# Optimization experiments

Hardware: AMD Instinct MI355X
Metric: run time of the kernel (lower is better)

## Reference

```python
import jax, jax.numpy as jnp
import numpy as np
from jax import lax

EPS = 1e-5
HEADS = 4
NPOINT = 512


def _layernorm(x, g, b):
    mu = jnp.mean(x, axis=-1, keepdims=True)
    var = jnp.var(x, axis=-1, keepdims=True)
    return (x - mu) * lax.rsqrt(var + EPS) * g + b


def farthest_point_sample(xyz, npoint):
    # xyz: [B, N, 3] -> idx [B, npoint]  (canonical PointNet++ FPS, seeded at point 0)
    B, N, _ = xyz.shape

    def step(carry, _):
        dist, far = carry  # [B,N], [B]
        centroid = jnp.take_along_axis(xyz, far[:, None, None], axis=1)  # [B,1,3]
        d = jnp.sum((xyz - centroid) ** 2, axis=-1)  # [B,N]
        dist = jnp.minimum(dist, d)
        nxt = jnp.argmax(dist, axis=1).astype(jnp.int32)
        return (dist, nxt), far

    init = (jnp.full((B, N), 1e10, xyz.dtype), jnp.zeros((B,), jnp.int32))
    _, idx = lax.scan(step, init, None, length=npoint)  # [npoint, B]
    return idx.T  # [B, npoint]


def index_points(points, idx):
    # points: [B, N, D], idx: [B, S] -> [B, S, D]
    return jnp.take_along_axis(points, idx[..., None], axis=1)


def setup_inputs() -> dict:
    key = jax.random.key(0)
    ks = iter(jax.random.split(key, 16))
    B, N, Cin, D, Dff, Dout = 8, 2048, 64, 128, 512, 256
    w = lambda k, s: (jax.random.normal(k, s, jnp.float32) * 0.02)
    inp = {
        "xyz": jax.random.normal(next(ks), (B, 3, N), jnp.float32),
        "points": jax.random.normal(next(ks), (B, Cin, N), jnp.float32),
        "W_proj": w(next(ks), (D, Cin)), "b_proj": jnp.zeros((D,)),
        "bn1_g": jnp.ones((D,)), "bn1_b": jnp.zeros((D,)),
        "bn1_m": jnp.zeros((D,)), "bn1_v": jnp.ones((D,)),
        "W_pos": w(next(ks), (D, 3)), "b_pos": jnp.zeros((D,)),
        "Wq": w(next(ks), (D, D)), "bq": jnp.zeros((D,)),
        "Wk": w(next(ks), (D, D)), "bk": jnp.zeros((D,)),
        "Wv": w(next(ks), (D, D)), "bv": jnp.zeros((D,)),
        "Wo": w(next(ks), (D, D)), "bo": jnp.zeros((D,)),
        "ln1_g": jnp.ones((D,)), "ln1_b": jnp.zeros((D,)),
        "W1": w(next(ks), (Dff, D)), "b1": jnp.zeros((Dff,)),
        "W2": w(next(ks), (D, Dff)), "b2": jnp.zeros((D,)),
        "ln2_g": jnp.ones((D,)), "ln2_b": jnp.zeros((D,)),
        "W_fc": w(next(ks), (Dout, D + 3)), "b_fc": jnp.zeros((Dout,)),
        "bn2_g": jnp.ones((Dout,)), "bn2_b": jnp.zeros((Dout,)),
        "bn2_m": jnp.zeros((Dout,)), "bn2_v": jnp.ones((Dout,)),
    }
    return inp


def reference(xyz, points, W_proj, b_proj, bn1_g, bn1_b, bn1_m, bn1_v,
              W_pos, b_pos, Wq, bq, Wk, bk, Wv, bv, Wo, bo,
              ln1_g, ln1_b, W1, b1, W2, b2, ln2_g, ln2_b,
              W_fc, b_fc, bn2_g, bn2_b, bn2_m, bn2_v):
    B, _, N = xyz.shape
    D = W_proj.shape[0]
    hd = D // HEADS

    # project: pointwise conv + BN (inference), output [B, N, D]
    feat = jnp.einsum('dc,bcn->bnd', W_proj, points) + b_proj
    feat = (feat - bn1_m) * lax.rsqrt(bn1_v + EPS) * bn1_g + bn1_b

    # transformer block with xyz positional encoding
    pos = jnp.einsum('dc,bcn->bnd', W_pos, xyz) + b_pos
    x = feat + pos
    q = (x @ Wq.T + bq).reshape(B, N, HEADS, hd)
    k = (x @ Wk.T + bk).reshape(B, N, HEADS, hd)
    v = (x @ Wv.T + bv).reshape(B, N, HEADS, hd)
    scores = jnp.einsum('bnhd,bmhd->bhnm', q, k) / jnp.sqrt(jnp.float32(hd))
    attn = jax.nn.softmax(scores, axis=-1)
    o = jnp.einsum('bhnm,bmhd->bnhd', attn, v).reshape(B, N, D)
    x = _layernorm(x + (o @ Wo.T + bo), ln1_g, ln1_b)
    ffn = jax.nn.relu(x @ W1.T + b1) @ W2.T + b2
    features = _layernorm(x + ffn, ln2_g, ln2_b)  # [B, N, D]

    # sampling + gather
    xyz_t = jnp.transpose(xyz, (0, 2, 1))  # [B, N, 3]
    fps_idx = farthest_point_sample(xyz_t, NPOINT)  # [B, npoint]
    new_points = index_points(features, fps_idx)    # [B, npoint, D]
    new_xyz = index_points(xyz_t, fps_idx)          # [B, npoint, 3]

    cat = jnp.concatenate([new_points, new_xyz], axis=-1)  # [B, npoint, D+3]
    out = jnp.einsum('od,bnd->bon', W_fc, cat) + b_fc[None, :, None]
    out = (out - bn2_m[None, :, None]) * lax.rsqrt(bn2_v + EPS)[None, :, None] \
          * bn2_g[None, :, None] + bn2_b[None, :, None]
    out = jax.nn.relu(out)  # [B, Dout, npoint]

    return jnp.transpose(new_xyz, (0, 2, 1)), out
```

## Files before the change

kernel.cpp:

```cpp
#include <hip/hip_runtime.h>
#include <hip/hip_bf16.h>

#define B_    8
#define N_    2048
#define CIN_  64
#define D_    128
#define DFF_  512
#define DOUT_ 256
#define S_    512
#define H_    4
#define HD_   32
#define EPS_  1e-5f

typedef unsigned short u16;
typedef unsigned long long u64;
typedef __attribute__((ext_vector_type(8))) short short8v;
typedef __attribute__((ext_vector_type(4))) float f32x4;

__device__ __forceinline__ u16 f2bu(float f) {
  __hip_bfloat16 h = __float2bfloat16(f);
  return *(u16*)&h;
}
__device__ __forceinline__ float bu2f(u16 u) {
  __hip_bfloat16 h = *(__hip_bfloat16*)&u;
  return __bfloat162float(h);
}

#define OW_QKV 0
#define OW_O   49152
#define OW_1   65536
#define OW_2   131072
#define OW_FC  196608
#define OW_CAT 237568
#define NW_TOT 249856

__global__ __launch_bounds__(256) void prep_kernel(
    const float* __restrict__ Wq, const float* __restrict__ bq,
    const float* __restrict__ Wk, const float* __restrict__ bk,
    const float* __restrict__ Wv, const float* __restrict__ bv,
    const float* __restrict__ Wo, const float* __restrict__ W1,
    const float* __restrict__ W2, const float* __restrict__ Wfc,
    const float* __restrict__ bfc, const float* __restrict__ Wp,
    const float* __restrict__ bp, const float* __restrict__ Wpos,
    const float* __restrict__ bpos, const float* __restrict__ g1,
    const float* __restrict__ be1, const float* __restrict__ m1,
    const float* __restrict__ v1, const float* __restrict__ g2,
    const float* __restrict__ bb2, const float* __restrict__ m2,
    const float* __restrict__ v2, u16* __restrict__ wb,
    float* __restrict__ fb) {
  const float SC = 0.1767766952966369f * 1.4426950408889634f;
  int i = blockIdx.x * 256 + threadIdx.x;
  if (i < OW_O) {
    int n = i >> 7, k = i & 127;
    float v = (n < 128) ? Wq[i] * SC
                        : (n < 256) ? Wk[(n - 128) * 128 + k]
                                    : Wv[(n - 256) * 128 + k];
    wb[OW_QKV + i] = f2bu(v);
  } else if (i < OW_1) {
    wb[i] = f2bu(Wo[i - OW_O]);
  } else if (i < OW_2) {
    wb[i] = f2bu(W1[i - OW_1]);
  } else if (i < OW_FC) {
    wb[i] = f2bu(W2[i - OW_2]);
  } else if (i < OW_CAT) {
    int j = i - OW_FC;
    int n = j / 160, c = j % 160;
    wb[i] = f2bu(c < 131 ? Wfc[n * 131 + c] : 0.f);
  } else if (i < NW_TOT) {
    int j = i - OW_CAT;
    int d = j / 96, c = j % 96;
    float v;
    if (c < 64) v = Wp[d * 64 + c] * (g1[d] * rsqrtf(v1[d] + EPS_));
    else if (c < 67) v = Wpos[d * 3 + (c - 64)];
    else v = 0.f;
    wb[i] = f2bu(v);
  } else if (i < NW_TOT + 384) {
    int n = i - NW_TOT;
    fb[n] = (n < 128) ? bq[n] * SC : (n < 256) ? bk[n - 128] : bv[n - 256];
  } else if (i < NW_TOT + 512) {
    int d = i - (NW_TOT + 384);
    float s1 = g1[d] * rsqrtf(v1[d] + EPS_);
    fb[384 + d] = (bp[d] - m1[d]) * s1 + be1[d] + bpos[d];
  } else if (i < NW_TOT + 768) {
    int n = i - (NW_TOT + 512);
    fb[512 + n] = g2[n] * rsqrtf(v2[n] + EPS_);
  } else if (i < NW_TOT + 1024) {
    int n = i - (NW_TOT + 768);
    float s = g2[n] * rsqrtf(v2[n] + EPS_);
    fb[768 + n] = bfc[n] * s + bb2[n] - m2[n] * s;
  }
}

#define FPS_SMEM 320

template <int CTRL, int RM>
__device__ __forceinline__ float dppmax(float v) {
  int m = __builtin_amdgcn_update_dpp(__float_as_int(v), __float_as_int(v),
                                      CTRL, RM, 0xF, true);
  return fmaxf(v, __int_as_float(m));
}

__device__ __forceinline__ void fps_slice(
    char* smem, int b, const float* __restrict__ xyz,
    float* __restrict__ dist_ws, int* __restrict__ far_ws,
    int* __restrict__ idx_out, float* __restrict__ out0, int s0, int s1) {
  u64* keys = (u64*)smem;
  float* crd = (float*)(smem + 64);
  __builtin_amdgcn_s_setprio(3);
  const int t = threadIdx.x, w = t >> 6, lane = t & 63;
  const float* xb = xyz + (size_t)b * 3 * N_;
  const int base = (w * 64 + lane) * 8;
  float* dw = dist_ws + b * N_;
  float px[8], py[8], pz[8], dist[8];
#pragma unroll
  for (int j = 0; j < 8; j++) {
    px[j] = xb[base + j];
    py[j] = xb[N_ + base + j];
    pz[j] = xb[2 * N_ + base + j];
    dist[j] = 1e10f;
  }
  if (s0 != 0) {
#pragma unroll
    for (int j = 0; j < 8; j++) dist[j] = dw[base + j];
  }
  int far = (s0 == 0) ? 0 : far_ws[b];
  float cx = xb[far], cy = xb[N_ + far], cz = xb[2 * N_ + far];
  for (int s = s0; s < s1; s++) {
    if (t == 0) {
      idx_out[b * S_ + s] = far;
      out0[(size_t)b * 3 * S_ + s] = cx;
      out0[(size_t)b * 3 * S_ + S_ + s] = cy;
      out0[(size_t)b * 3 * S_ + 2 * S_ + s] = cz;
    }
    float best = -1.0f, bx = 0.f, by = 0.f, bz = 0.f;
    int bestp = 0;
#pragma unroll
    for (int j = 0; j < 8; j++) {
      float dx = __fsub_rn(px[j], cx);
      float dy = __fsub_rn(py[j], cy);
      float dz = __fsub_rn(pz[j], cz);
      float d = __fadd_rn(__fadd_rn(__fmul_rn(dx, dx), __fmul_rn(dy, dy)),
                          __fmul_rn(dz, dz));
      float nd = fminf(dist[j], d);
      dist[j] = nd;
      if (nd > best) {
        best = nd; bestp = base + j;
        bx = px[j]; by = py[j]; bz = pz[j];
      }
    }
    float m = best;
    m = dppmax<0x111, 0xF>(m);
    m = dppmax<0x112, 0xF>(m);
    m = dppmax<0x114, 0xF>(m);
    m = dppmax<0x118, 0xF>(m);
    m = dppmax<0x142, 0xA>(m);
    m = dppmax<0x143, 0xC>(m);
    float M = __int_as_float(__builtin_amdgcn_readlane(__float_as_int(m), 63));
    u64 mask = __ballot(best == M);
    int wl = __ffsll((long long)mask) - 1;
    if (lane == wl) {
      int sb = (s & 1) * 4 + w;
      keys[sb] = ((u64)__float_as_uint(M) << 32) |
                 (unsigned)(0xFFFFFFFFu - (unsigned)bestp);
      crd[sb * 3 + 0] = bx;
      crd[sb * 3 + 1] = by;
      crd[sb * 3 + 2] = bz;
    }
    asm volatile("s_waitcnt lgkmcnt(0)" ::: "memory");
    __builtin_amdgcn_s_barrier();
    asm volatile("" ::: "memory");
    const int q0 = (s & 1) * 4;
    u64 kk = keys[q0];
    float ccx = crd[q0 * 3], ccy = crd[q0 * 3 + 1], ccz = crd[q0 * 3 + 2];
#pragma unroll
    for (int i = 1; i < 4; i++) {
      u64 ki = keys[q0 + i];
      bool c = ki > kk;
      kk = c ? ki : kk;
      ccx = c ? crd[(q0 + i) * 3] : ccx;
      ccy = c ? crd[(q0 + i) * 3 + 1] : ccy;
      ccz = c ? crd[(q0 + i) * 3 + 2] : ccz;
    }
    far = (int)(0xFFFFFFFFu - (unsigned)kk);
    cx = ccx; cy = ccy; cz = ccz;
  }
#pragma unroll
  for (int j = 0; j < 8; j++) dw[base + j] = dist[j];
  if (t == 0) far_ws[b] = far;
  __builtin_amdgcn_s_setprio(0);
}

template <int K, int KC, int ASTAGE, int EPI>
__global__ __launch_bounds__(256) void gemm_k(
    const u16* __restrict__ A, const u16* __restrict__ W,
    const float* __restrict__ srcf0, const float* __restrict__ srcf1,
    const int* __restrict__ fidx, const float* __restrict__ p0,
    const float* __restrict__ p1, const float* __restrict__ p2,
    const u16* __restrict__ resid, u16* __restrict__ outb,
    float* __restrict__ outf, int ntn, int fpsnb, int s0, int s1,
    const float* fxyz, float* fdist, int* ffar, int* fidxo, float* fout0) {
  constexpr int KP = KC + 8;
  constexpr int GEMM_SMEM = 2 * 128 * KP * 2;
  constexpr int SMEM = GEMM_SMEM > FPS_SMEM ? GEMM_SMEM : FPS_SMEM;
  __shared__ __align__(16) char smem[SMEM];
  if ((int)blockIdx.x < fpsnb) {
    fps_slice(smem, blockIdx.x, fxyz, fdist, ffar, fidxo, fout0, s0, s1);
    return;
  }
  u16 (*As)[KP] = (u16 (*)[KP])smem;
  u16 (*Ws)[KP] = (u16 (*)[KP])(smem + 128 * KP * 2);
  const int bid = blockIdx.x - fpsnb;
  const int mt = bid / ntn, nt = bid % ntn;
  const int t = threadIdx.x, w = t >> 6, lane = t & 63;
  const int g = lane >> 4, lr = lane & 15;

  f32x4 acc[2][8];
#pragma unroll
  for (int qf = 0; qf < 2; qf++)
#pragma unroll
    for (int nf = 0; nf < 8; nf++) acc[qf][nf] = {0.f, 0.f, 0.f, 0.f};

  for (int kc = 0; kc < K / KC; kc++) {
    __syncthreads();
    for (int i = t; i < 128 * (KC / 8); i += 256) {
      int row = i / (KC / 8), c8 = i % (KC / 8);
      *(short8v*)&Ws[row][c8 * 8] =
          *(const short8v*)(W + (size_t)(nt * 128 + row) * K + kc * KC + c8 * 8);
    }
    if constexpr (ASTAGE == 0) {
      for (int i = t; i < 128 * (KC / 8); i += 256) {
        int row = i / (KC / 8), c8 = i % (KC / 8);
        *(short8v*)&As[row][c8 * 8] =
            *(const short8v*)(A + (size_t)(mt * 128 + row) * K + kc * KC + c8 * 8);
      }
    } else if constexpr (ASTAGE == 1) {
      int bb = (mt * 128) >> 11, n0 = (mt * 128) & (N_ - 1);
      for (int i = t; i < 96 * 128; i += 256) {
        int c = i >> 7, n = i & 127;
        float v;
        if (c < 64) v = srcf0[((size_t)bb * CIN_ + c) * N_ + n0 + n];
        else if (c < 67) v = srcf1[((size_t)bb * 3 + (c - 64)) * N_ + n0 + n];
        else v = 0.f;
        As[n][c] = f2bu(v);
      }
    } else {
      int bb = (mt * 128) >> 9, sq0 = (mt * 128) & (S_ - 1);
      for (int i = t; i < 128 * 20; i += 256) {
        int row = i / 20, c8 = i % 20;
        int id = fidx[bb * S_ + sq0 + row];
        short8v val;
        if (c8 < 16) {
          val = *(const short8v*)(A + ((size_t)bb * N_ + id) * D_ + c8 * 8);
        } else if (c8 == 16) {
          val = short8v{0, 0, 0, 0, 0, 0, 0, 0};
          val[0] = (short)f2bu(srcf1[((size_t)bb * 3 + 0) * N_ + id]);
          val[1] = (short)f2bu(srcf1[((size_t)bb * 3 + 1) * N_ + id]);
          val[2] = (short)f2bu(srcf1[((size_t)bb * 3 + 2) * N_ + id]);
        } else {
          val = short8v{0, 0, 0, 0, 0, 0, 0, 0};
        }
        *(short8v*)&As[row][c8 * 8] = val;
      }
    }
    __syncthreads();
#pragma unroll
    for (int ks = 0; ks < KC / 32; ks++) {
      short8v a0 = *(const short8v*)&As[w * 32 + lr][ks * 32 + 8 * g];
      short8v a1 = *(const short8v*)&As[w * 32 + 16 + lr][ks * 32 + 8 * g];
#pragma unroll
      for (int nf = 0; nf < 8; nf++) {
        short8v bb = *(const short8v*)&Ws[nf * 16 + lr][ks * 32 + 8 * g];
        acc[0][nf] = __builtin_amdgcn_mfma_f32_16x16x32_bf16(a0, bb, acc[0][nf], 0, 0, 0);
        acc[1][nf] = __builtin_amdgcn_mfma_f32_16x16x32_bf16(a1, bb, acc[1][nf], 0, 0, 0);
      }
    }
  }

  if constexpr (EPI == 3) {
#pragma unroll
    for (int qf = 0; qf < 2; qf++) {
#pragma unroll
      for (int i = 0; i < 4; i++) {
        int m = mt * 128 + w * 32 + qf * 16 + 4 * g + i;
        float v[8], sm = 0.f, sq = 0.f;
#pragma unroll
        for (int nf = 0; nf < 8; nf++) {
          int n = nf * 16 + lr;
          float x = acc[qf][nf][i] + p0[n] + bu2f(resid[(size_t)m * D_ + n]);
          v[nf] = x;
          sm += x;
          sq += x * x;
        }
#pragma unroll
        for (int msk = 1; msk < 16; msk <<= 1) {
          sm += __shfl_xor(sm, msk);
          sq += __shfl_xor(sq, msk);
        }
        float mu = sm * (1.f / 128.f);
        float var = sq * (1.f / 128.f) - mu * mu;
        float rs = rsqrtf(var + EPS_);
#pragma unroll
        for (int nf = 0; nf < 8; nf++) {
          int n = nf * 16 + lr;
          outb[(size_t)m * D_ + n] = f2bu((v[nf] - mu) * rs * p1[n] + p2[n]);
        }
      }
    }
  } else {
#pragma unroll
    for (int qf = 0; qf < 2; qf++)
#pragma unroll
      for (int nf = 0; nf < 8; nf++)
#pragma unroll
        for (int i = 0; i < 4; i++) {
          int m = mt * 128 + w * 32 + qf * 16 + 4 * g + i;
          int nl = nf * 16 + lr;
          int n = nt * 128 + nl;
          float vv = acc[qf][nf][i];
          if constexpr (EPI == 0) {
            outb[(size_t)m * D_ + nl] = f2bu(vv + p0[n]);
          } else if constexpr (EPI == 1) {
            vv += p0[n];
            int which = n >> 7, h = (n >> 5) & 3, c = n & 31;
            int bb = m >> 11, tok = m & (N_ - 1);
            outb[(size_t)which * 2097152 +
                 (((size_t)bb * H_ + h) * N_ + tok) * HD_ + c] = f2bu(vv);
          } else if constexpr (EPI == 2) {
            outb[(size_t)m * DFF_ + n] = f2bu(fmaxf(vv + p0[n], 0.f));
          } else {
            float r = fmaxf(vv * p1[n] + p2[n], 0.f);
            outf[((size_t)(m >> 9) * DOUT_ + n) * S_ + (m & (S_ - 1))] = r;
          }
        }
  }
}

__global__ __launch_bounds__(256) void attn_mfma_kernel(
    const u16* __restrict__ qg, const u16* __restrict__ kg,
    const u16* __restrict__ vg, u16* __restrict__ o, int fpsnb, int s0, int s1,
    const float* fxyz, float* fdist, int* ffar, int* fidxo, float* fout0) {
  constexpr int ATTN_SMEM = 64 * 40 * 2 + 32 * 72 * 2 + 4 * 16 * 72 * 2;
  constexpr int SMEM = ATTN_SMEM > FPS_SMEM ? ATTN_SMEM : FPS_SMEM;
  __shared__ __align__(16) char smem[SMEM];
  if ((int)blockIdx.x < fpsnb) {
    fps_slice(smem, blockIdx.x, fxyz, fdist, ffar, fidxo, fout0, s0, s1);
    return;
  }
  const int t = threadIdx.x;
  const int w = t >> 6, lane = t & 63, g = lane >> 4, lr = lane & 15;
  u16 (*ks)[40] = (u16 (*)[40])smem;
  u16 (*vt)[72] = (u16 (*)[72])(smem + 5120);
  u16 (*psw)[72] = (u16 (*)[72])(smem + 9728) + w * 16;

  const int bid = blockIdx.x - fpsnb;
  const int qt = bid & 31;
  const int bh = bid >> 5;
  const int b = bh >> 2, h = bh & 3;
  const int qrow = qt * 64 + w * 16 + lr;

  short8v aq = *(const short8v*)(qg + ((size_t)bh * N_ + qrow) * HD_ + 8 * g);

  const u16* kb = kg + (size_t)bh * N_ * HD_;
  const u16* vb = vg + (size_t)bh * N_ * HD_;

  const f32x4 fzero = {0.f, 0.f, 0.f, 0.f};
  float mrun = -INFINITY, lrun = 0.f;
  f32x4 acco[2] = {fzero, fzero};

  const int srow = t >> 2, scol = (t & 3) * 8;

  for (int ch = 0; ch < 32; ch++) {
    __syncthreads();
    short8v kvv = *(const short8v*)(kb + (size_t)(ch * 64 + srow) * HD_ + scol);
    short8v vvv = *(const short8v*)(vb + (size_t)(ch * 64 + srow) * HD_ + scol);
    *(short8v*)(&ks[srow][scol]) = kvv;
#pragma unroll
    for (int e = 0; e < 8; e++) vt[scol + e][srow] = (u16)vvv[e];
    __syncthreads();

    f32x4 stv[4];
#pragma unroll
    for (int kt = 0; kt < 4; kt++) {
      short8v ak = *(const short8v*)(&ks[kt * 16 + lr][8 * g]);
      stv[kt] = __builtin_amdgcn_mfma_f32_16x16x32_bf16(ak, aq, fzero, 0, 0, 0);
    }

    float mx = -INFINITY;
#pragma unroll
    for (int kt = 0; kt < 4; kt++)
#pragma unroll
      for (int i = 0; i < 4; i++) mx = fmaxf(mx, stv[kt][i]);
    mx = fmaxf(mx, __shfl_xor(mx, 16));
    mx = fmaxf(mx, __shfl_xor(mx, 32));
    float nm = fmaxf(mrun, mx);
    float alpha = exp2f(mrun - nm);
    mrun = nm;
    float psum = 0.f;
#pragma unroll
    for (int kt = 0; kt < 4; kt++) {
      float p0 = exp2f(stv[kt][0] - nm);
      float p1 = exp2f(stv[kt][1] - nm);
      float p2 = exp2f(stv[kt][2] - nm);
      float p3 = exp2f(stv[kt][3] - nm);
      psum += (p0 + p1) + (p2 + p3);
      u64 pk = (u64)f2bu(p0) | ((u64)f2bu(p1) << 16) |
               ((u64)f2bu(p2) << 32) | ((u64)f2bu(p3) << 48);
      *(u64*)(&psw[lr][kt * 16 + 4 * g]) = pk;
    }
    psum += __shfl_xor(psum, 16);
    psum += __shfl_xor(psum, 32);
    lrun = lrun * alpha + psum;
#pragma unroll
    for (int dt = 0; dt < 2; dt++)
#pragma unroll
      for (int i = 0; i < 4; i++) acco[dt][i] *= alpha;

#pragma unroll
    for (int mc = 0; mc < 2; mc++) {
      short8v pb = *(const short8v*)(&psw[lr][mc * 32 + 8 * g]);
#pragma unroll
      for (int dt = 0; dt < 2; dt++) {
        short8v av = *(const short8v*)(&vt[dt * 16 + lr][mc * 32 + 8 * g]);
        acco[dt] = __builtin_amdgcn_mfma_f32_16x16x32_bf16(av, pb, acco[dt], 0, 0, 0);
      }
    }
  }

  float rl = 1.0f / lrun;
#pragma unroll
  for (int dt = 0; dt < 2; dt++) {
    u64 pk = (u64)f2bu(acco[dt][0] * rl) | ((u64)f2bu(acco[dt][1] * rl) << 16) |
             ((u64)f2bu(acco[dt][2] * rl) << 32) |
             ((u64)f2bu(acco[dt][3] * rl) << 48);
    *(u64*)(o + ((size_t)b * N_ + qrow) * D_ + h * HD_ + dt * 16 + 4 * g) = pk;
  }
}

extern "C" void kernel_launch(void* const* d_in, const int* in_sizes, int n_in,
                              void* d_out, int out_size, void* d_ws, size_t ws_size,
                              hipStream_t stream) {
  const float* xyz    = (const float*)d_in[0];
  const float* points = (const float*)d_in[1];
  const float* Wp     = (const float*)d_in[2];
  const float* bp     = (const float*)d_in[3];
  const float* g1     = (const float*)d_in[4];
  const float* be1    = (const float*)d_in[5];
  const float* m1     = (const float*)d_in[6];
  const float* v1     = (const float*)d_in[7];
  const float* Wpos   = (const float*)d_in[8];
  const float* bpos   = (const float*)d_in[9];
  const float* Wq     = (const float*)d_in[10];
  const float* bq     = (const float*)d_in[11];
  const float* Wk     = (const float*)d_in[12];
  const float* bk     = (const float*)d_in[13];
  const float* Wv     = (const float*)d_in[14];
  const float* bv     = (const float*)d_in[15];
  const float* Wo     = (const float*)d_in[16];
  const float* bo     = (const float*)d_in[17];
  const float* lg1    = (const float*)d_in[18];
  const float* lb1    = (const float*)d_in[19];
  const float* W1     = (const float*)d_in[20];
  const float* b1     = (const float*)d_in[21];
  const float* W2     = (const float*)d_in[22];
  const float* b2p    = (const float*)d_in[23];
  const float* lg2    = (const float*)d_in[24];
  const float* lb2    = (const float*)d_in[25];
  const float* Wfc    = (const float*)d_in[26];
  const float* bfc    = (const float*)d_in[27];
  const float* g2     = (const float*)d_in[28];
  const float* bb2    = (const float*)d_in[29];
  const float* m2     = (const float*)d_in[30];
  const float* v2     = (const float*)d_in[31];

  float* out0 = (float*)d_out;
  float* out1 = out0 + (size_t)B_ * 3 * S_;

  char* ws = (char*)d_ws;
  int*   fps_idx = (int*)ws;
  u16*   wb      = (u16*)(ws + 16384);
  float* fb      = (float*)(ws + 516096);
  float* dist_ws = (float*)(ws + 520192);
  int*   far_ws  = (int*)(ws + 585728);
  const size_t MB = 1024 * 1024;
  u16* x     = (u16*)(ws + 1 * MB);
  u16* o     = (u16*)(ws + 5 * MB);
  u16* x2    = (u16*)(ws + 9 * MB);
  u16* feats = (u16*)(ws + 13 * MB);
  u16* qb    = (u16*)(ws + 17 * MB);
  u16* h     = (u16*)(ws + 29 * MB);

  prep_kernel<<<980, 256, 0, stream>>>(Wq, bq, Wk, bk, Wv, bv, Wo, W1, W2, Wfc,
                                       bfc, Wp, bp, Wpos, bpos, g1, be1, m1, v1,
                                       g2, bb2, m2, v2, wb, fb);

  gemm_k<96, 96, 1, 0><<<8 + 128, 256, 0, stream>>>(
      nullptr, wb + OW_CAT, points, xyz, nullptr, fb + 384, nullptr, nullptr,
      nullptr, x, nullptr, 1, 8, 0, 48, xyz, dist_ws, far_ws, fps_idx, out0);
  gemm_k<128, 128, 0, 1><<<8 + 384, 256, 0, stream>>>(
      x, wb + OW_QKV, nullptr, nullptr, nullptr, fb, nullptr, nullptr,
      nullptr, qb, nullptr, 3, 8, 48, 136, xyz, dist_ws, far_ws, fps_idx, out0);
  attn_mfma_kernel<<<8 + B_ * H_ * (N_ / 64), 256, 0, stream>>>(
      qb, qb + 2097152, qb + 2 * 2097152, o, 8, 136, 236, xyz, dist_ws, far_ws,
      fps_idx, out0);
  gemm_k<128, 128, 0, 3><<<8 + 128, 256, 0, stream>>>(
      o, wb + OW_O, nullptr, nullptr, nullptr, bo, lg1, lb1, x, x2, nullptr, 1,
      8, 236, 320, xyz, dist_ws, far_ws, fps_idx, out0);
  gemm_k<128, 128, 0, 2><<<8 + 512, 256, 0, stream>>>(
      x2, wb + OW_1, nullptr, nullptr, nullptr, b1, nullptr, nullptr,
      nullptr, h, nullptr, 4, 8, 320, 420, xyz, dist_ws, far_ws, fps_idx, out0);
  gemm_k<512, 128, 0, 3><<<8 + 128, 256, 0, stream>>>(
      h, wb + OW_2, nullptr, nullptr, nullptr, b2p, lg2, lb2, x2, feats,
      nullptr, 1, 8, 420, 512, xyz, dist_ws, far_ws, fps_idx, out0);
  gemm_k<160, 160, 2, 4><<<64, 256, 0, stream>>>(
      feats, wb + OW_FC, nullptr, xyz, fps_idx, nullptr, fb + 512, fb + 768,
      nullptr, nullptr, out1, 2, 0, 0, 0, nullptr, nullptr, nullptr, nullptr,
      nullptr);
}
```

Measured before the change: 397.5 us.

## Store V transposed from QKV GEMM, drop FPS priority, rebalance FPS slices

After: 385.1 us. 1.03x faster.

```diff
diff --git a/kernel.cpp b/kernel.cpp
--- a/kernel.cpp
+++ b/kernel.cpp
@@ -106,7 +106,6 @@
     int* __restrict__ idx_out, float* __restrict__ out0, int s0, int s1) {
   u64* keys = (u64*)smem;
   float* crd = (float*)(smem + 64);
-  __builtin_amdgcn_s_setprio(3);
   const int t = threadIdx.x, w = t >> 6, lane = t & 63;
   const float* xb = xyz + (size_t)b * 3 * N_;
   const int base = (w * 64 + lane) * 8;
@@ -187,7 +186,6 @@
 #pragma unroll
   for (int j = 0; j < 8; j++) dw[base + j] = dist[j];
   if (t == 0) far_ws[b] = far;
-  __builtin_amdgcn_s_setprio(0);
 }
 
 template <int K, int KC, int ASTAGE, int EPI>
@@ -306,6 +304,44 @@
         }
       }
     }
+  } else if constexpr (EPI == 1) {
+    if (nt < 2) {
+#pragma unroll
+      for (int qf = 0; qf < 2; qf++)
+#pragma unroll
+        for (int nf = 0; nf < 8; nf++)
+#pragma unroll
+          for (int i = 0; i < 4; i++) {
+            int m = mt * 128 + w * 32 + qf * 16 + 4 * g + i;
+            int n = nt * 128 + nf * 16 + lr;
+            float vv = acc[qf][nf][i] + p0[n];
+            int hh = (n >> 5) & 3, c = n & 31;
+            int bb = m >> 11, tok = m & (N_ - 1);
+            outb[(size_t)nt * 2097152 +
+                 (((size_t)bb * H_ + hh) * N_ + tok) * HD_ + c] = f2bu(vv);
+          }
+    } else {
+      __syncthreads();
+      u16 (*Vt)[KP] = (u16 (*)[KP])smem;
+#pragma unroll
+      for (int qf = 0; qf < 2; qf++)
+#pragma unroll
+        for (int nf = 0; nf < 8; nf++)
+#pragma unroll
+          for (int i = 0; i < 4; i++) {
+            int m_l = w * 32 + qf * 16 + 4 * g + i;
+            int n_l = nf * 16 + lr;
+            Vt[n_l][m_l] = f2bu(acc[qf][nf][i] + p0[256 + n_l]);
+          }
+      __syncthreads();
+      int bb = (mt * 128) >> 11, tok0 = (mt * 128) & (N_ - 1);
+      for (int i2 = t; i2 < 2048; i2 += 256) {
+        int row = i2 >> 4, seg = i2 & 15;
+        *(short8v*)(outb + (size_t)2 * 2097152 +
+                    (((size_t)bb * H_ + (row >> 5)) * HD_ + (row & 31)) * N_ +
+                    tok0 + seg * 8) = *(const short8v*)&Vt[row][seg * 8];
+      }
+    }
   } else {
 #pragma unroll
     for (int qf = 0; qf < 2; qf++)
@@ -319,12 +355,6 @@
           float vv = acc[qf][nf][i];
           if constexpr (EPI == 0) {
             outb[(size_t)m * D_ + nl] = f2bu(vv + p0[n]);
-          } else if constexpr (EPI == 1) {
-            vv += p0[n];
-            int which = n >> 7, h = (n >> 5) & 3, c = n & 31;
-            int bb = m >> 11, tok = m & (N_ - 1);
-            outb[(size_t)which * 2097152 +
-                 (((size_t)bb * H_ + h) * N_ + tok) * HD_ + c] = f2bu(vv);
           } else if constexpr (EPI == 2) {
             outb[(size_t)m * DFF_ + n] = f2bu(fmaxf(vv + p0[n], 0.f));
           } else {
@@ -361,21 +391,21 @@
   short8v aq = *(const short8v*)(qg + ((size_t)bh * N_ + qrow) * HD_ + 8 * g);
 
   const u16* kb = kg + (size_t)bh * N_ * HD_;
-  const u16* vb = vg + (size_t)bh * N_ * HD_;
+  const u16* vbt = vg + (size_t)bh * N_ * HD_;
 
   const f32x4 fzero = {0.f, 0.f, 0.f, 0.f};
   float mrun = -INFINITY, lrun = 0.f;
   f32x4 acco[2] = {fzero, fzero};
 
-  const int srow = t >> 2, scol = (t & 3) * 8;
+  const int krow = t >> 2, kseg = (t & 3) * 8;
+  const int vrow = t >> 3, vseg = (t & 7) * 8;
 
   for (int ch = 0; ch < 32; ch++) {
     __syncthreads();
-    short8v kvv = *(const short8v*)(kb + (size_t)(ch * 64 + srow) * HD_ + scol);
-    short8v vvv = *(const short8v*)(vb + (size_t)(ch * 64 + srow) * HD_ + scol);
-    *(short8v*)(&ks[srow][scol]) = kvv;
-#pragma unroll
-    for (int e = 0; e < 8; e++) vt[scol + e][srow] = (u16)vvv[e];
+    *(short8v*)(&ks[krow][kseg]) =
+        *(const short8v*)(kb + (size_t)(ch * 64 + krow) * HD_ + kseg);
+    *(short8v*)(&vt[vrow][vseg]) =
+        *(const short8v*)(vbt + (size_t)vrow * N_ + ch * 64 + vseg);
     __syncthreads();
 
     f32x4 stv[4];
@@ -495,22 +525,22 @@
 
   gemm_k<96, 96, 1, 0><<<8 + 128, 256, 0, stream>>>(
       nullptr, wb + OW_CAT, points, xyz, nullptr, fb + 384, nullptr, nullptr,
-      nullptr, x, nullptr, 1, 8, 0, 48, xyz, dist_ws, far_ws, fps_idx, out0);
+      nullptr, x, nullptr, 1, 8, 0, 64, xyz, dist_ws, far_ws, fps_idx, out0);
   gemm_k<128, 128, 0, 1><<<8 + 384, 256, 0, stream>>>(
       x, wb + OW_QKV, nullptr, nullptr, nullptr, fb, nullptr, nullptr,
-      nullptr, qb, nullptr, 3, 8, 48, 136, xyz, dist_ws, far_ws, fps_idx, out0);
+      nullptr, qb, nullptr, 3, 8, 64, 156, xyz, dist_ws, far_ws, fps_idx, out0);
   attn_mfma_kernel<<<8 + B_ * H_ * (N_ / 64), 256, 0, stream>>>(
-      qb, qb + 2097152, qb + 2 * 2097152, o, 8, 136, 236, xyz, dist_ws, far_ws,
+      qb, qb + 2097152, qb + 2 * 2097152, o, 8, 156, 264, xyz, dist_ws, far_ws,
       fps_idx, out0);
   gemm_k<128, 128, 0, 3><<<8 + 128, 256, 0, stream>>>(
       o, wb + OW_O, nullptr, nullptr, nullptr, bo, lg1, lb1, x, x2, nullptr, 1,
-      8, 236, 320, xyz, dist_ws, far_ws, fps_idx, out0);
+      8, 264, 336, xyz, dist_ws, far_ws, fps_idx, out0);
   gemm_k<128, 128, 0, 2><<<8 + 512, 256, 0, stream>>>(
       x2, wb + OW_1, nullptr, nullptr, nullptr, b1, nullptr, nullptr,
-      nullptr, h, nullptr, 4, 8, 320, 420, xyz, dist_ws, far_ws, fps_idx, out0);
+      nullptr, h, nullptr, 4, 8, 336, 440, xyz, dist_ws, far_ws, fps_idx, out0);
   gemm_k<512, 128, 0, 3><<<8 + 128, 256, 0, stream>>>(
       h, wb + OW_2, nullptr, nullptr, nullptr, b2p, lg2, lb2, x2, feats,
-      nullptr, 1, 8, 420, 512, xyz, dist_ws, far_ws, fps_idx, out0);
+      nullptr, 1, 8, 440, 512, xyz, dist_ws, far_ws, fps_idx, out0);
   gemm_k<160, 160, 2, 4><<<64, 256, 0, stream>>>(
       feats, wb + OW_FC, nullptr, xyz, fps_idx, nullptr, fb + 512, fb + 768,
       nullptr, nullptr, out1, 2, 0, 0, 0, nullptr, nullptr, nullptr, nullptr,
```
